# Performance work log

Hardware: AMD Instinct MI355X
Metric: run time of the kernel (lower is better)

Reference implementation:

```python
import jax, jax.numpy as jnp
import numpy as np

D_MODEL = 1024
NUM_LAYERS = 4
D_STATE = 64
D_CONV = 4
EXPAND = 2
HEADDIM = 64  # headdim = d_state per the module
D_INNER = EXPAND * D_MODEL              # 2048
NHEADS = D_INNER // HEADDIM             # 32
CONV_DIM = D_INNER + 2 * D_STATE        # 2176 (x, B, C)
D_IN_PROJ = 2 * D_INNER + 2 * D_STATE + NHEADS  # 4384 (z, xBC, dt)
EPS = 1e-5


def setup_inputs() -> dict:
    key = jax.random.key(0)
    ks = jax.random.split(key, 8)
    B, L = 4, 2048
    x = jax.random.normal(ks[0], (B, L, D_MODEL), dtype=jnp.float32)
    # stacked per-layer parameters
    in_w = jax.random.normal(ks[1], (NUM_LAYERS, D_MODEL, D_IN_PROJ), dtype=jnp.float32) * 0.02
    conv_w = (jax.random.uniform(ks[2], (NUM_LAYERS, D_CONV, CONV_DIM), dtype=jnp.float32) - 0.5) * (2.0 / np.sqrt(D_CONV))
    conv_b = jnp.zeros((NUM_LAYERS, CONV_DIM), dtype=jnp.float32)
    # dt init as in mamba-ssm: dt ~ exp(U * (log(0.1)-log(0.001)) + log(0.001)), dt_bias = inv_softplus(dt)
    u = jax.random.uniform(ks[3], (NUM_LAYERS, NHEADS), dtype=jnp.float32)
    dt = jnp.exp(u * (np.log(0.1) - np.log(0.001)) + np.log(0.001))
    dt_bias = dt + jnp.log(-jnp.expm1(-dt))
    A_log = jnp.log(jax.random.uniform(ks[4], (NUM_LAYERS, NHEADS), dtype=jnp.float32, minval=1.0, maxval=16.0))
    Dp = jnp.ones((NUM_LAYERS, NHEADS), dtype=jnp.float32)
    norm_w = jnp.ones((NUM_LAYERS, D_INNER), dtype=jnp.float32)
    out_w = jax.random.normal(ks[5], (NUM_LAYERS, D_INNER, D_MODEL), dtype=jnp.float32) * 0.02
    ln_w = jnp.ones((NUM_LAYERS, D_MODEL), dtype=jnp.float32)
    ln_b = jnp.zeros((NUM_LAYERS, D_MODEL), dtype=jnp.float32)
    return {"x": x, "ln_w": ln_w, "ln_b": ln_b, "in_w": in_w, "conv_w": conv_w,
            "conv_b": conv_b, "dt_bias": dt_bias, "A_log": A_log, "Dp": Dp,
            "norm_w": norm_w, "out_w": out_w}


def _layernorm(x, w, b):
    mu = jnp.mean(x, axis=-1, keepdims=True)
    xc = x - mu
    var = jnp.mean(xc * xc, axis=-1, keepdims=True)
    return xc * jax.lax.rsqrt(var + EPS) * w + b


def _mamba2(x, in_w, conv_w, conv_b, dt_bias, A_log, Dp, norm_w, out_w):
    Bb, L, _ = x.shape
    zxbcdt = jnp.einsum('bld,de->ble', x, in_w)            # (B,L,D_IN_PROJ)
    z = zxbcdt[..., :D_INNER]                               # (B,L,D_INNER)
    xBC = zxbcdt[..., D_INNER:D_INNER + CONV_DIM]           # (B,L,CONV_DIM)
    dt = jax.nn.softplus(zxbcdt[..., -NHEADS:] + dt_bias)   # (B,L,H)
    # causal depthwise conv1d (kernel D_CONV) + SiLU
    xp = jnp.pad(xBC, ((0, 0), (D_CONV - 1, 0), (0, 0)))
    conv = conv_b + sum(xp[:, k:k + L, :] * conv_w[k] for k in range(D_CONV))
    xBC = jax.nn.silu(conv)
    xs = xBC[..., :D_INNER].reshape(Bb, L, NHEADS, HEADDIM)  # (B,L,H,P)
    Bm = xBC[..., D_INNER:D_INNER + D_STATE]                 # (B,L,N), ngroups=1
    Cm = xBC[..., D_INNER + D_STATE:]                        # (B,L,N)
    A = -jnp.exp(A_log)                                      # (H,)
    dA = jnp.exp(dt * A)                                     # (B,L,H) decay per step
    dBx = dt[..., None] * xs                                 # (B,L,H,P)
    # selective state-space scan: h_t = dA_t*h_{t-1} + dBx_t (x) B_t ; y_t = h_t . C_t
    def step(h, t_in):
        dA_t, dBx_t, B_t, C_t = t_in
        h = h * dA_t[:, :, None, None] + dBx_t[..., None] * B_t[:, None, None, :]
        y = jnp.einsum('bhpn,bn->bhp', h, C_t)
        return h, y
    h0 = jnp.zeros((Bb, NHEADS, HEADDIM, D_STATE), x.dtype)
    xsT = (jnp.moveaxis(dA, 1, 0), jnp.moveaxis(dBx, 1, 0),
           jnp.moveaxis(Bm, 1, 0), jnp.moveaxis(Cm, 1, 0))
    _, yT = jax.lax.scan(step, h0, xsT)
    y = jnp.moveaxis(yT, 0, 1)                               # (B,L,H,P)
    y = y + Dp[None, None, :, None] * xs                     # skip via per-head D
    y = y.reshape(Bb, L, D_INNER)
    # gated RMSNorm (norm_before_gate=False): rmsnorm(y * silu(z)) * w
    y = y * jax.nn.silu(z)
    y = y * jax.lax.rsqrt(jnp.mean(y * y, axis=-1, keepdims=True) + EPS) * norm_w
    return jnp.einsum('ble,ed->bld', y, out_w)


def reference(x, ln_w, ln_b, in_w, conv_w, conv_b, dt_bias, A_log, Dp, norm_w, out_w):
    for i in range(NUM_LAYERS):
        xn = _layernorm(x, ln_w[i], ln_b[i])
        x = x + _mamba2(xn, in_w[i], conv_w[i], conv_b[i], dt_bias[i],
                        A_log[i], Dp[i], norm_w[i], out_w[i])
    return x
```

## Files before the change

### kernel.cpp

```cpp
#include <hip/hip_runtime.h>
#include <math.h>

#define LSEQ   2048
#define NROWS  8192
#define DMODEL 1024
#define DINNER 2048
#define NH     32
#define CONVD  2176
#define NPROJ  4256
#define NPROJ_PAD 4352
#define EPSV   1e-5f
#define SEGS   16
#define TSEG   128

typedef __bf16 bf16x8_t __attribute__((ext_vector_type(8)));
typedef float f32x4_t __attribute__((ext_vector_type(4)));
typedef unsigned short u16x8_t __attribute__((ext_vector_type(8)));

__device__ __forceinline__ unsigned short f2bf(float f) {
  unsigned int u = __float_as_uint(f);
  u += 0x7fffu + ((u >> 16) & 1u);
  return (unsigned short)(u >> 16);
}
__device__ __forceinline__ float bf2f(unsigned short u) {
  return __uint_as_float((unsigned int)u << 16);
}
__device__ __forceinline__ float siluf(float x) { return x / (1.f + expf(-x)); }

__global__ __launch_bounds__(256) void ln_kernel(const float* __restrict__ X,
    const float* __restrict__ w, const float* __restrict__ b,
    unsigned short* __restrict__ out)
{
  const int r = blockIdx.x, tid = threadIdx.x;
  __shared__ float red[4];
  const float4 v = ((const float4*)(X + (size_t)r * DMODEL))[tid];
  float s = v.x + v.y + v.z + v.w;
#pragma unroll
  for (int o = 32; o > 0; o >>= 1) s += __shfl_down(s, o);
  if ((tid & 63) == 0) red[tid >> 6] = s;
  __syncthreads();
  const float mu = (red[0] + red[1] + red[2] + red[3]) * (1.f / DMODEL);
  __syncthreads();
  const float dx = v.x - mu, dy = v.y - mu, dz = v.z - mu, dw = v.w - mu;
  float ss = dx * dx + dy * dy + dz * dz + dw * dw;
#pragma unroll
  for (int o = 32; o > 0; o >>= 1) ss += __shfl_down(ss, o);
  if ((tid & 63) == 0) red[tid >> 6] = ss;
  __syncthreads();
  const float var = (red[0] + red[1] + red[2] + red[3]) * (1.f / DMODEL);
  const float rs = rsqrtf(var + EPSV);
  const float4 wv = ((const float4*)w)[tid];
  const float4 bv = ((const float4*)b)[tid];
  const size_t d = (size_t)r * DMODEL + tid * 4;
  out[d + 0] = f2bf(dx * rs * wv.x + bv.x);
  out[d + 1] = f2bf(dy * rs * wv.y + bv.y);
  out[d + 2] = f2bf(dz * rs * wv.z + bv.z);
  out[d + 3] = f2bf(dw * rs * wv.w + bv.w);
}

__global__ void transpose_bf16(const float* __restrict__ W,
    unsigned short* __restrict__ WT, int K, int N)
{
  __shared__ float t[32][33];
  const int n0 = blockIdx.x * 32, k0 = blockIdx.y * 32;
  const int tx = threadIdx.x, ty = threadIdx.y;
  if (n0 + tx < N) t[ty][tx] = W[(size_t)(k0 + ty) * N + n0 + tx];
  __syncthreads();
  if (n0 + ty < N) WT[(size_t)(n0 + ty) * K + k0 + tx] = f2bf(t[tx][ty]);
}

__global__ __launch_bounds__(256) void gemm_bf16(
    const unsigned short* __restrict__ A,
    const unsigned short* __restrict__ BT,
    float* __restrict__ Cf,
    unsigned short* __restrict__ Cb,
    int N, int K, int ldc)
{
  __shared__ unsigned short sA[128 * 32];
  __shared__ unsigned short sB[128 * 32];
  const int tid = threadIdx.x;
  const int w = tid >> 6, l = tid & 63;
  const int wr = w >> 1, wc = w & 1;
  const int la = l & 15, lb = l >> 4;
  const int m0 = blockIdx.x * 128, n0 = blockIdx.y * 128;
  f32x4_t acc[4][4];
#pragma unroll
  for (int i = 0; i < 4; ++i)
#pragma unroll
    for (int j = 0; j < 4; ++j) acc[i][j] = (f32x4_t){0.f, 0.f, 0.f, 0.f};

  const int r0 = tid >> 2, q0 = tid & 3;
  for (int kt = 0; kt < K; kt += 32) {
    const u16x8_t a0 = *(const u16x8_t*)(A + (size_t)(m0 + r0) * K + kt + q0 * 8);
    const u16x8_t a1 = *(const u16x8_t*)(A + (size_t)(m0 + r0 + 64) * K + kt + q0 * 8);
    const u16x8_t b0 = *(const u16x8_t*)(BT + (size_t)(n0 + r0) * K + kt + q0 * 8);
    const u16x8_t b1 = *(const u16x8_t*)(BT + (size_t)(n0 + r0 + 64) * K + kt + q0 * 8);
    __syncthreads();
    *(u16x8_t*)(sA + tid * 8) = a0;
    *(u16x8_t*)(sA + 2048 + tid * 8) = a1;
    *(u16x8_t*)(sB + tid * 8) = b0;
    *(u16x8_t*)(sB + 2048 + tid * 8) = b1;
    __syncthreads();
    bf16x8_t af[4], bfr[4];
#pragma unroll
    for (int mi = 0; mi < 4; ++mi)
      af[mi] = *(const bf16x8_t*)(sA + (wr * 64 + mi * 16 + la) * 32 + lb * 8);
#pragma unroll
    for (int ni = 0; ni < 4; ++ni)
      bfr[ni] = *(const bf16x8_t*)(sB + (wc * 64 + ni * 16 + la) * 32 + lb * 8);
#pragma unroll
    for (int mi = 0; mi < 4; ++mi)
#pragma unroll
      for (int ni = 0; ni < 4; ++ni)
        acc[mi][ni] = __builtin_amdgcn_mfma_f32_16x16x32_bf16(af[mi], bfr[ni], acc[mi][ni], 0, 0, 0);
  }
#pragma unroll
  for (int mi = 0; mi < 4; ++mi) {
#pragma unroll
    for (int ni = 0; ni < 4; ++ni) {
      const int col = n0 + wc * 64 + ni * 16 + la;
      if (col < N) {
#pragma unroll
        for (int r = 0; r < 4; ++r) {
          const int row = m0 + wr * 64 + mi * 16 + lb * 4 + r;
          const size_t idx = (size_t)row * ldc + col;
          const float v = acc[mi][ni][r];
          if (Cb) Cb[idx] = f2bf(v);
          else    Cf[idx] += v;
        }
      }
    }
  }
}

__global__ __launch_bounds__(256) void dt_kernel(const unsigned short* __restrict__ zx,
    const float* __restrict__ dt_bias, const float* __restrict__ A_log,
    float* __restrict__ dt, float* __restrict__ ldA)
{
  const int i = blockIdx.x * 256 + threadIdx.x;
  const int r = i >> 5, h = i & 31;
  const float xr = bf2f(zx[(size_t)r * NPROJ + (DINNER + CONVD) + h]) + dt_bias[h];
  const float dtv = (xr > 20.f) ? xr : log1pf(expf(xr));
  dt[i] = dtv;
  ldA[i] = -dtv * expf(A_log[h]);
}

__global__ __launch_bounds__(256) void conv_kernel(const unsigned short* __restrict__ zx,
    const float* __restrict__ cw, const float* __restrict__ cb,
    unsigned short* __restrict__ out)
{
  const int c = blockIdx.x * 256 + threadIdx.x;
  if (c >= CONVD) return;
  const int r = blockIdx.y;
  const int l = r & (LSEQ - 1);
  float acc = cb[c];
#pragma unroll
  for (int k = 0; k < 4; ++k) {
    const int ls = l + k - 3;
    if (ls >= 0)
      acc = fmaf(bf2f(zx[(size_t)(r + k - 3) * NPROJ + DINNER + c]), cw[k * CONVD + c], acc);
  }
  out[(size_t)r * CONVD + c] = f2bf(siluf(acc));
}

#define CBB(t, cbyte)  ((char*)CB  + (t) * 256 + ((cbyte) ^ (((t) & 7) << 4)))
#define XTB(p, cbyte)  ((char*)Xt  + (p) * 256 + ((cbyte) ^ (((p) & 7) << 4)))
#define BTWB(n, cbyte) ((char*)Btw + (n) * 256 + ((cbyte) ^ (((n) & 7) << 4)))
__global__ __launch_bounds__(256) void ssd_chunk_kernel(
    const unsigned short* __restrict__ xbc,
    const float* __restrict__ dtb,
    const float* __restrict__ ldA,
    const float* __restrict__ Dp,
    unsigned short* __restrict__ y, int ldy,
    unsigned short* __restrict__ H,
    float* __restrict__ cumdec)
{
  __shared__ unsigned short CB[TSEG * 128];
  __shared__ unsigned short Xt[64 * TSEG];
  __shared__ unsigned short Btw[64 * TSEG];
  __shared__ float cumS[TSEG], dtS[TSEG], wS[TSEG];
  const int id = blockIdx.x;
  const int bh = id >> 4, ch = id & 15;
  const int b = bh >> 5, h = bh & 31;
  const int tid = threadIdx.x;
  const int w = tid >> 6, l = tid & 63;
  const int la = l & 15, lb = l >> 4;
  const size_t row0 = (size_t)b * LSEQ + (size_t)ch * TSEG;
  const unsigned short* xr = xbc + row0 * CONVD;
  const float dp = Dp[h];

  {
    const int t = tid >> 1, q = tid & 1;
    const unsigned short* src = xr + (size_t)t * CONVD;
#pragma unroll
    for (int j = 0; j < 4; ++j) {
      const int c0 = q * 32 + j * 8;
      *(u16x8_t*)CBB(t, c0 * 2)       = *(const u16x8_t*)(src + 2112 + c0);
      *(u16x8_t*)CBB(t, 128 + c0 * 2) = *(const u16x8_t*)(src + 2048 + c0);
      const u16x8_t xv = *(const u16x8_t*)(src + h * 64 + c0);
#pragma unroll
      for (int e = 0; e < 8; ++e)
        *(unsigned short*)XTB(c0 + e, t * 2) = xv[e];
    }
  }
  if (w == 0) {
    float a0 = ldA[(row0 + l) * NH + h];
    float a1 = ldA[(row0 + 64 + l) * NH + h];
    const float d0 = dtb[(row0 + l) * NH + h];
    const float d1 = dtb[(row0 + 64 + l) * NH + h];
#pragma unroll
    for (int o = 1; o < 64; o <<= 1) { const float u = __shfl_up(a0, o); if (l >= o) a0 += u; }
    const float tot0 = __shfl(a0, 63);
#pragma unroll
    for (int o = 1; o < 64; o <<= 1) { const float u = __shfl_up(a1, o); if (l >= o) a1 += u; }
    a1 += tot0;
    const float cT = __shfl(a1, 63);
    cumS[l] = a0;       cumS[64 + l] = a1;
    dtS[l] = d0;        dtS[64 + l] = d1;
    wS[l] = __expf(cT - a0) * d0;
    wS[64 + l] = __expf(cT - a1) * d1;
    float* cdg = cumdec + (size_t)bh * LSEQ + (size_t)ch * TSEG;
    cdg[l] = __expf(a0);
    cdg[64 + l] = __expf(a1);
  }
  __syncthreads();

  f32x4_t g[2][8];
#pragma unroll
  for (int mi = 0; mi < 2; ++mi)
#pragma unroll
    for (int ni = 0; ni < 8; ++ni) g[mi][ni] = (f32x4_t){0.f, 0.f, 0.f, 0.f};
#pragma unroll
  for (int ks = 0; ks < 2; ++ks) {
    bf16x8_t af[2], bfr[8];
#pragma unroll
    for (int mi = 0; mi < 2; ++mi)
      af[mi] = *(const bf16x8_t*)CBB(w * 32 + mi * 16 + la, ks * 64 + lb * 16);
#pragma unroll
    for (int ni = 0; ni < 8; ++ni)
      bfr[ni] = *(const bf16x8_t*)CBB(ni * 16 + la, 128 + ks * 64 + lb * 16);
#pragma unroll
    for (int mi = 0; mi < 2; ++mi)
#pragma unroll
      for (int ni = 0; ni < 8; ++ni)
        g[mi][ni] = __builtin_amdgcn_mfma_f32_16x16x32_bf16(af[mi], bfr[ni], g[mi][ni], 0, 0, 0);
  }
  __syncthreads();

#pragma unroll
  for (int mi = 0; mi < 2; ++mi) {
#pragma unroll
    for (int ni = 0; ni < 8; ++ni) {
      const int s = ni * 16 + la;
#pragma unroll
      for (int r = 0; r < 4; ++r) {
        const int t = w * 32 + mi * 16 + lb * 4 + r;
        float mv = 0.f;
        if (s <= t) mv = g[mi][ni][r] * __expf(cumS[t] - cumS[s]) * dtS[s];
        if (s == t) mv += dp;
        *(unsigned short*)CBB(t, s * 2) = f2bf(mv);
      }
    }
  }
  {
    const int s = tid >> 1, q = tid & 1;
    const unsigned short* src = xr + (size_t)s * CONVD + 2048;
    const float ww = wS[s];
#pragma unroll
    for (int j = 0; j < 4; ++j) {
      const int c0 = q * 32 + j * 8;
      const u16x8_t bv = *(const u16x8_t*)(src + c0);
#pragma unroll
      for (int e = 0; e < 8; ++e)
        *(unsigned short*)BTWB(c0 + e, s * 2) = f2bf(bf2f(bv[e]) * ww);
    }
  }
  __syncthreads();

  f32x4_t y1[2][4];
#pragma unroll
  for (int mi = 0; mi < 2; ++mi)
#pragma unroll
    for (int ni = 0; ni < 4; ++ni) y1[mi][ni] = (f32x4_t){0.f, 0.f, 0.f, 0.f};
#pragma unroll
  for (int ks = 0; ks < 4; ++ks) {
    bf16x8_t af[2], xf[4];
#pragma unroll
    for (int mi = 0; mi < 2; ++mi)
      af[mi] = *(const bf16x8_t*)CBB(w * 32 + mi * 16 + la, ks * 64 + lb * 16);
#pragma unroll
    for (int ni = 0; ni < 4; ++ni)
      xf[ni] = *(const bf16x8_t*)XTB(ni * 16 + la, ks * 64 + lb * 16);
#pragma unroll
    for (int mi = 0; mi < 2; ++mi)
#pragma unroll
      for (int ni = 0; ni < 4; ++ni)
        y1[mi][ni] = __builtin_amdgcn_mfma_f32_16x16x32_bf16(af[mi], xf[ni], y1[mi][ni], 0, 0, 0);
  }
  f32x4_t hacc[4];
#pragma unroll
  for (int ni = 0; ni < 4; ++ni) hacc[ni] = (f32x4_t){0.f, 0.f, 0.f, 0.f};
#pragma unroll
  for (int ks = 0; ks < 4; ++ks) {
    const bf16x8_t af = *(const bf16x8_t*)XTB(w * 16 + la, ks * 64 + lb * 16);
    bf16x8_t bw[4];
#pragma unroll
    for (int ni = 0; ni < 4; ++ni)
      bw[ni] = *(const bf16x8_t*)BTWB(ni * 16 + la, ks * 64 + lb * 16);
#pragma unroll
    for (int ni = 0; ni < 4; ++ni)
      hacc[ni] = __builtin_amdgcn_mfma_f32_16x16x32_bf16(af, bw[ni], hacc[ni], 0, 0, 0);
  }

  unsigned short* yg = y + row0 * ldy + h * 64;
#pragma unroll
  for (int mi = 0; mi < 2; ++mi)
#pragma unroll
    for (int ni = 0; ni < 4; ++ni)
#pragma unroll
      for (int r = 0; r < 4; ++r) {
        const int t = w * 32 + mi * 16 + lb * 4 + r;
        yg[(size_t)t * ldy + ni * 16 + la] = f2bf(y1[mi][ni][r]);
      }
  unsigned short* Hg = H + ((size_t)ch * 128 + bh) * 4096;
#pragma unroll
  for (int ni = 0; ni < 4; ++ni)
#pragma unroll
    for (int r = 0; r < 4; ++r) {
      const int p = w * 16 + lb * 4 + r;
      Hg[p * 64 + ni * 16 + la] = f2bf(hacc[ni][r]);
    }
}

__global__ __launch_bounds__(256) void scan2_kernel(
    unsigned short* __restrict__ H, const float* __restrict__ cumdec)
{
  const int bh = blockIdx.x;
  const int e = threadIdx.x * 16;
  float hs[16];
#pragma unroll
  for (int k = 0; k < 16; ++k) hs[k] = 0.f;
  unsigned short* Hb = H + (size_t)bh * 4096 + e;
  const float* cd = cumdec + (size_t)bh * LSEQ;
  for (int s = 0; s < SEGS; ++s) {
    unsigned short* p = Hb + (size_t)s * 128 * 4096;
    const float rseg = cd[s * TSEG + TSEG - 1];
    u16x8_t v0 = *(u16x8_t*)p, v1 = *(u16x8_t*)(p + 8);
    u16x8_t w0, w1;
#pragma unroll
    for (int k = 0; k < 8; ++k) {
      const float tmp = bf2f(v0[k]);
      w0[k] = f2bf(hs[k]);
      hs[k] = fmaf(rseg, hs[k], tmp);
    }
#pragma unroll
    for (int k = 0; k < 8; ++k) {
      const float tmp = bf2f(v1[k]);
      w1[k] = f2bf(hs[k + 8]);
      hs[k + 8] = fmaf(rseg, hs[k + 8], tmp);
    }
    *(u16x8_t*)p = w0;
    *(u16x8_t*)(p + 8) = w1;
  }
}

#define CSB(t, cbyte) ((char*)Cs + (t) * 128 + ((cbyte) ^ (((t) & 7) << 4)))
#define HSB(p, cbyte) ((char*)Hs + (p) * 128 + ((cbyte) ^ (((p) & 7) << 4)))
__global__ __launch_bounds__(256) void scan3_mfma(
    const unsigned short* __restrict__ xbc,
    const float* __restrict__ cumdec,
    const unsigned short* __restrict__ H,
    unsigned short* __restrict__ y, int ldy)
{
  __shared__ unsigned short Cs[TSEG * 64];
  __shared__ unsigned short Hs[64 * 64];
  __shared__ float cdS[TSEG];
  const int id = blockIdx.x;
  const int bh = id / 15, ch = id % 15 + 1;
  const int b = bh >> 5, h = bh & 31;
  const int tid = threadIdx.x, w = tid >> 6, l = tid & 63;
  const int la = l & 15, lb = l >> 4;
  const size_t row0 = (size_t)b * LSEQ + (size_t)ch * TSEG;
  const unsigned short* xr = xbc + row0 * CONVD;
  {
    const int t = tid >> 1, q = tid & 1;
#pragma unroll
    for (int j = 0; j < 4; ++j) {
      const int c0 = q * 32 + j * 8;
      *(u16x8_t*)CSB(t, c0 * 2) = *(const u16x8_t*)(xr + (size_t)t * CONVD + 2112 + c0);
    }
  }
  {
    const int p = tid >> 2, q = tid & 3;
    const unsigned short* hsrc = H + ((size_t)ch * 128 + bh) * 4096 + p * 64;
#pragma unroll
    for (int j = 0; j < 2; ++j) {
      const int c0 = q * 16 + j * 8;
      *(u16x8_t*)HSB(p, c0 * 2) = *(const u16x8_t*)(hsrc + c0);
    }
  }
  if (tid < TSEG) cdS[tid] = cumdec[(size_t)bh * LSEQ + (size_t)ch * TSEG + tid];
  __syncthreads();
  f32x4_t acc[2][4];
#pragma unroll
  for (int mi = 0; mi < 2; ++mi)
#pragma unroll
    for (int ni = 0; ni < 4; ++ni) acc[mi][ni] = (f32x4_t){0.f, 0.f, 0.f, 0.f};
#pragma unroll
  for (int ks = 0; ks < 2; ++ks) {
    bf16x8_t af[2], bfr[4];
#pragma unroll
    for (int mi = 0; mi < 2; ++mi)
      af[mi] = *(const bf16x8_t*)CSB(w * 32 + mi * 16 + la, ks * 64 + lb * 16);
#pragma unroll
    for (int ni = 0; ni < 4; ++ni)
      bfr[ni] = *(const bf16x8_t*)HSB(ni * 16 + la, ks * 64 + lb * 16);
#pragma unroll
    for (int mi = 0; mi < 2; ++mi)
#pragma unroll
      for (int ni = 0; ni < 4; ++ni)
        acc[mi][ni] = __builtin_amdgcn_mfma_f32_16x16x32_bf16(af[mi], bfr[ni], acc[mi][ni], 0, 0, 0);
  }
  unsigned short* yg = y + row0 * ldy + h * 64;
#pragma unroll
  for (int mi = 0; mi < 2; ++mi)
#pragma unroll
    for (int ni = 0; ni < 4; ++ni)
#pragma unroll
      for (int r = 0; r < 4; ++r) {
        const int t = w * 32 + mi * 16 + lb * 4 + r;
        unsigned short* yp = yg + (size_t)t * ldy + ni * 16 + la;
        *yp = f2bf(bf2f(*yp) + acc[mi][ni][r] * cdS[t]);
      }
}

__global__ __launch_bounds__(256) void gate_kernel(const unsigned short* __restrict__ zx,
    const float* __restrict__ nw, unsigned short* __restrict__ out)
{
  const int r = blockIdx.x, tid = threadIdx.x;
  __shared__ float red[4];
  const size_t rb = (size_t)r * NPROJ;
  const u16x8_t zv = *(const u16x8_t*)(zx + rb + tid * 8);
  const u16x8_t yv = *(const u16x8_t*)(zx + rb + 2048 + tid * 8);
  float v[8];
#pragma unroll
  for (int i = 0; i < 8; ++i) v[i] = bf2f(yv[i]) * siluf(bf2f(zv[i]));
  float ss = 0.f;
#pragma unroll
  for (int i = 0; i < 8; ++i) ss += v[i] * v[i];
#pragma unroll
  for (int o = 32; o > 0; o >>= 1) ss += __shfl_down(ss, o);
  if ((tid & 63) == 0) red[tid >> 6] = ss;
  __syncthreads();
  const float var = (red[0] + red[1] + red[2] + red[3]) * (1.f / DINNER);
  const float rs = rsqrtf(var + EPSV);
  const float4 w0 = ((const float4*)nw)[tid * 2];
  const float4 w1 = ((const float4*)nw)[tid * 2 + 1];
  u16x8_t o;
  o[0] = f2bf(v[0] * rs * w0.x); o[1] = f2bf(v[1] * rs * w0.y);
  o[2] = f2bf(v[2] * rs * w0.z); o[3] = f2bf(v[3] * rs * w0.w);
  o[4] = f2bf(v[4] * rs * w1.x); o[5] = f2bf(v[5] * rs * w1.y);
  o[6] = f2bf(v[6] * rs * w1.z); o[7] = f2bf(v[7] * rs * w1.w);
  *(u16x8_t*)(out + (size_t)r * DINNER + tid * 8) = o;
}

extern "C" void kernel_launch(void* const* d_in, const int* in_sizes, int n_in,
                              void* d_out, int out_size, void* d_ws, size_t ws_size,
                              hipStream_t stream) {
  (void)in_sizes; (void)n_in; (void)out_size; (void)ws_size;
  const float* x_in    = (const float*)d_in[0];
  const float* ln_w    = (const float*)d_in[1];
  const float* ln_b    = (const float*)d_in[2];
  const float* in_w    = (const float*)d_in[3];
  const float* conv_w  = (const float*)d_in[4];
  const float* conv_b  = (const float*)d_in[5];
  const float* dt_bias = (const float*)d_in[6];
  const float* A_log   = (const float*)d_in[7];
  const float* Dp      = (const float*)d_in[8];
  const float* norm_w  = (const float*)d_in[9];
  const float* out_w   = (const float*)d_in[10];
  float* xout = (float*)d_out;

  char* ws = (char*)d_ws;
  unsigned short* zxb  = (unsigned short*)ws;
  char* r1 = ws + (size_t)NROWS * NPROJ * 2;
  unsigned short* xn   = (unsigned short*)r1;
  unsigned short* xbcb = (unsigned short*)r1;
  unsigned short* ybf  = (unsigned short*)r1;
  char* wth = r1 + (size_t)NROWS * CONVD * 2;
  unsigned short* inwT = (unsigned short*)wth;
  unsigned short* owT  = (unsigned short*)wth;
  unsigned short* Hbuf = (unsigned short*)wth;
  float* dtb = (float*)(wth + (size_t)SEGS * 128 * 4096 * 2);
  float* ldAb = dtb + (size_t)NROWS * NH;
  float* cumdec = ldAb + (size_t)NROWS * NH;

  hipMemcpyAsync(xout, x_in, (size_t)NROWS * DMODEL * 4, hipMemcpyDeviceToDevice, stream);

  for (int i = 0; i < 4; ++i) {
    ln_kernel<<<NROWS, 256, 0, stream>>>(xout, ln_w + i * DMODEL, ln_b + i * DMODEL, xn);
    transpose_bf16<<<dim3(133, 32), dim3(32, 32), 0, stream>>>(
        in_w + (size_t)i * DMODEL * NPROJ, inwT, DMODEL, NPROJ);
    gemm_bf16<<<dim3(64, 34), 256, 0, stream>>>(xn, inwT, nullptr, zxb, NPROJ, DMODEL, NPROJ);
    dt_kernel<<<(NROWS * NH) / 256, 256, 0, stream>>>(zxb, dt_bias + i * NH, A_log + i * NH, dtb, ldAb);
    conv_kernel<<<dim3(9, NROWS), 256, 0, stream>>>(
        zxb, conv_w + (size_t)i * 4 * CONVD, conv_b + i * CONVD, xbcb);
    ssd_chunk_kernel<<<128 * SEGS, 256, 0, stream>>>(xbcb, dtb, ldAb, Dp + i * NH,
                                                     zxb + 2048, NPROJ, Hbuf, cumdec);
    scan2_kernel<<<128, 256, 0, stream>>>(Hbuf, cumdec);
    scan3_mfma<<<128 * 15, 256, 0, stream>>>(xbcb, cumdec, Hbuf, zxb + 2048, NPROJ);
    gate_kernel<<<NROWS, 256, 0, stream>>>(zxb, norm_w + i * DINNER, ybf);
    transpose_bf16<<<dim3(32, 64), dim3(32, 32), 0, stream>>>(
        out_w + (size_t)i * DINNER * DMODEL, owT, DINNER, DMODEL);
    gemm_bf16<<<dim3(64, 8), 256, 0, stream>>>(ybf, owT, xout, nullptr, DMODEL, DINNER, DMODEL);
  }
}
```

Before: 1.576 ms.

## Load GEMM tiles directly to LDS, vectorize conv, fuse dt into SSD chunk

The bf16 GEMM now stages its A and B tiles with global_load_lds, writing 16 bytes per lane straight into shared memory instead of going through registers. The depthwise conv kernel handles 8 channels per thread with 16-byte vector loads and stores, so it launches far fewer threads. The separate dt/softplus kernel is removed: the SSD chunk kernel now computes dt and log-decay inline from the raw projection output, which drops one launch and the dt and ldA buffers. The risks are that correctness depends on the compiler handling the LDS base and the wait before the barrier, and that the GEMM main loop still has no double buffering.

```diff
diff --git a/kernel.cpp b/kernel.cpp
--- a/kernel.cpp
+++ b/kernel.cpp
@@ -27,6 +27,12 @@
 }
 __device__ __forceinline__ float siluf(float x) { return x / (1.f + expf(-x)); }
 
+__device__ __forceinline__ void gload16(const unsigned short* g, unsigned short* l) {
+  __builtin_amdgcn_global_load_lds(
+      (const __attribute__((address_space(1))) void*)g,
+      (__attribute__((address_space(3))) void*)l, 16, 0, 0);
+}
+
 __global__ __launch_bounds__(256) void ln_kernel(const float* __restrict__ X,
     const float* __restrict__ w, const float* __restrict__ b,
     unsigned short* __restrict__ out)
@@ -90,16 +96,15 @@
     for (int j = 0; j < 4; ++j) acc[i][j] = (f32x4_t){0.f, 0.f, 0.f, 0.f};
 
   const int r0 = tid >> 2, q0 = tid & 3;
+  const unsigned short* Ag = A + (size_t)(m0 + r0) * K + q0 * 8;
+  const unsigned short* Bg = BT + (size_t)(n0 + r0) * K + q0 * 8;
+
   for (int kt = 0; kt < K; kt += 32) {
-    const u16x8_t a0 = *(const u16x8_t*)(A + (size_t)(m0 + r0) * K + kt + q0 * 8);
-    const u16x8_t a1 = *(const u16x8_t*)(A + (size_t)(m0 + r0 + 64) * K + kt + q0 * 8);
-    const u16x8_t b0 = *(const u16x8_t*)(BT + (size_t)(n0 + r0) * K + kt + q0 * 8);
-    const u16x8_t b1 = *(const u16x8_t*)(BT + (size_t)(n0 + r0 + 64) * K + kt + q0 * 8);
     __syncthreads();
-    *(u16x8_t*)(sA + tid * 8) = a0;
-    *(u16x8_t*)(sA + 2048 + tid * 8) = a1;
-    *(u16x8_t*)(sB + tid * 8) = b0;
-    *(u16x8_t*)(sB + 2048 + tid * 8) = b1;
+    gload16(Ag + kt,                   sA + tid * 8);
+    gload16(Ag + (size_t)64 * K + kt,  sA + 2048 + tid * 8);
+    gload16(Bg + kt,                   sB + tid * 8);
+    gload16(Bg + (size_t)64 * K + kt,  sB + 2048 + tid * 8);
     __syncthreads();
     bf16x8_t af[4], bfr[4];
 #pragma unroll
@@ -133,34 +138,41 @@
   }
 }
 
-__global__ __launch_bounds__(256) void dt_kernel(const unsigned short* __restrict__ zx,
-    const float* __restrict__ dt_bias, const float* __restrict__ A_log,
-    float* __restrict__ dt, float* __restrict__ ldA)
-{
-  const int i = blockIdx.x * 256 + threadIdx.x;
-  const int r = i >> 5, h = i & 31;
-  const float xr = bf2f(zx[(size_t)r * NPROJ + (DINNER + CONVD) + h]) + dt_bias[h];
-  const float dtv = (xr > 20.f) ? xr : log1pf(expf(xr));
-  dt[i] = dtv;
-  ldA[i] = -dtv * expf(A_log[h]);
-}
-
 __global__ __launch_bounds__(256) void conv_kernel(const unsigned short* __restrict__ zx,
     const float* __restrict__ cw, const float* __restrict__ cb,
     unsigned short* __restrict__ out)
 {
-  const int c = blockIdx.x * 256 + threadIdx.x;
-  if (c >= CONVD) return;
+  const int c8 = (blockIdx.x * 256 + threadIdx.x) * 8;
+  if (c8 >= CONVD) return;
   const int r = blockIdx.y;
   const int l = r & (LSEQ - 1);
-  float acc = cb[c];
+  float acc[8];
+  {
+    const float4 b0 = *(const float4*)(cb + c8);
+    const float4 b1 = *(const float4*)(cb + c8 + 4);
+    acc[0] = b0.x; acc[1] = b0.y; acc[2] = b0.z; acc[3] = b0.w;
+    acc[4] = b1.x; acc[5] = b1.y; acc[6] = b1.z; acc[7] = b1.w;
+  }
 #pragma unroll
   for (int k = 0; k < 4; ++k) {
-    const int ls = l + k - 3;
-    if (ls >= 0)
-      acc = fmaf(bf2f(zx[(size_t)(r + k - 3) * NPROJ + DINNER + c]), cw[k * CONVD + c], acc);
-  }
-  out[(size_t)r * CONVD + c] = f2bf(siluf(acc));
+    if (l + k - 3 >= 0) {
+      const u16x8_t v = *(const u16x8_t*)(zx + (size_t)(r + k - 3) * NPROJ + DINNER + c8);
+      const float4 w0 = *(const float4*)(cw + k * CONVD + c8);
+      const float4 w1 = *(const float4*)(cw + k * CONVD + c8 + 4);
+      acc[0] = fmaf(bf2f(v[0]), w0.x, acc[0]);
+      acc[1] = fmaf(bf2f(v[1]), w0.y, acc[1]);
+      acc[2] = fmaf(bf2f(v[2]), w0.z, acc[2]);
+      acc[3] = fmaf(bf2f(v[3]), w0.w, acc[3]);
+      acc[4] = fmaf(bf2f(v[4]), w1.x, acc[4]);
+      acc[5] = fmaf(bf2f(v[5]), w1.y, acc[5]);
+      acc[6] = fmaf(bf2f(v[6]), w1.z, acc[6]);
+      acc[7] = fmaf(bf2f(v[7]), w1.w, acc[7]);
+    }
+  }
+  u16x8_t o;
+#pragma unroll
+  for (int j = 0; j < 8; ++j) o[j] = f2bf(siluf(acc[j]));
+  *(u16x8_t*)(out + (size_t)r * CONVD + c8) = o;
 }
 
 #define CBB(t, cbyte)  ((char*)CB  + (t) * 256 + ((cbyte) ^ (((t) & 7) << 4)))
@@ -168,8 +180,9 @@
 #define BTWB(n, cbyte) ((char*)Btw + (n) * 256 + ((cbyte) ^ (((n) & 7) << 4)))
 __global__ __launch_bounds__(256) void ssd_chunk_kernel(
     const unsigned short* __restrict__ xbc,
-    const float* __restrict__ dtb,
-    const float* __restrict__ ldA,
+    const unsigned short* __restrict__ zraw,
+    const float* __restrict__ dt_bias,
+    const float* __restrict__ A_log,
     const float* __restrict__ Dp,
     unsigned short* __restrict__ y, int ldy,
     unsigned short* __restrict__ H,
@@ -204,10 +217,14 @@
     }
   }
   if (w == 0) {
-    float a0 = ldA[(row0 + l) * NH + h];
-    float a1 = ldA[(row0 + 64 + l) * NH + h];
-    const float d0 = dtb[(row0 + l) * NH + h];
-    const float d1 = dtb[(row0 + 64 + l) * NH + h];
+    const float bias = dt_bias[h];
+    const float aexp = __expf(A_log[h]);
+    const float x0 = bf2f(zraw[(row0 + l) * NPROJ + (DINNER + CONVD) + h]) + bias;
+    const float x1 = bf2f(zraw[(row0 + 64 + l) * NPROJ + (DINNER + CONVD) + h]) + bias;
+    const float d0 = (x0 > 20.f) ? x0 : log1pf(__expf(x0));
+    const float d1 = (x1 > 20.f) ? x1 : log1pf(__expf(x1));
+    float a0 = -d0 * aexp;
+    float a1 = -d1 * aexp;
 #pragma unroll
     for (int o = 1; o < 64; o <<= 1) { const float u = __shfl_up(a0, o); if (l >= o) a0 += u; }
     const float tot0 = __shfl(a0, 63);
@@ -491,9 +508,7 @@
   unsigned short* inwT = (unsigned short*)wth;
   unsigned short* owT  = (unsigned short*)wth;
   unsigned short* Hbuf = (unsigned short*)wth;
-  float* dtb = (float*)(wth + (size_t)SEGS * 128 * 4096 * 2);
-  float* ldAb = dtb + (size_t)NROWS * NH;
-  float* cumdec = ldAb + (size_t)NROWS * NH;
+  float* cumdec = (float*)(wth + (size_t)SEGS * 128 * 4096 * 2);
 
   hipMemcpyAsync(xout, x_in, (size_t)NROWS * DMODEL * 4, hipMemcpyDeviceToDevice, stream);
 
@@ -502,11 +517,11 @@
     transpose_bf16<<<dim3(133, 32), dim3(32, 32), 0, stream>>>(
         in_w + (size_t)i * DMODEL * NPROJ, inwT, DMODEL, NPROJ);
     gemm_bf16<<<dim3(64, 34), 256, 0, stream>>>(xn, inwT, nullptr, zxb, NPROJ, DMODEL, NPROJ);
-    dt_kernel<<<(NROWS * NH) / 256, 256, 0, stream>>>(zxb, dt_bias + i * NH, A_log + i * NH, dtb, ldAb);
-    conv_kernel<<<dim3(9, NROWS), 256, 0, stream>>>(
+    conv_kernel<<<dim3(2, NROWS), 256, 0, stream>>>(
         zxb, conv_w + (size_t)i * 4 * CONVD, conv_b + i * CONVD, xbcb);
-    ssd_chunk_kernel<<<128 * SEGS, 256, 0, stream>>>(xbcb, dtb, ldAb, Dp + i * NH,
-                                                     zxb + 2048, NPROJ, Hbuf, cumdec);
+    ssd_chunk_kernel<<<128 * SEGS, 256, 0, stream>>>(xbcb, zxb,
+        dt_bias + i * NH, A_log + i * NH, Dp + i * NH,
+        zxb + 2048, NPROJ, Hbuf, cumdec);
     scan2_kernel<<<128, 256, 0, stream>>>(Hbuf, cumdec);
     scan3_mfma<<<128 * 15, 256, 0, stream>>>(xbcb, cumdec, Hbuf, zxb + 2048, NPROJ);
     gate_kernel<<<NROWS, 256, 0, stream>>>(zxb, norm_w + i * DINNER, ybf);
```

Result: faster. 1.414 ms (-10.3%).
